# Kernel tuning notes

Hardware: AMD Instinct MI355X
Metric: run time of the kernel (lower is better)

## Reference

```python
import jax, jax.numpy as jnp
import numpy as np

LAMBDA_B = 5.0
N = 16_777_216  # 2^24 samples -> ~128 MB of fp32 inputs


def setup_inputs() -> dict:
    key = jax.random.key(0)
    k1, k2 = jax.random.split(key)
    y_true = jax.random.uniform(k1, (N,), dtype=jnp.float32)  # IWI-like scores in [0,1)
    y_pred = y_true + 0.1 * jax.random.normal(k2, (N,), dtype=jnp.float32)
    quants = jnp.arange(6, dtype=jnp.float32) / 5.0  # [0.0, 0.2, ..., 1.0]
    return {"y_pred": y_pred, "y_true": y_true, "quants": quants}


def reference(y_pred, y_true, quants):
    # MSE term
    diff = y_pred - y_true
    mse = jnp.mean(diff * diff)

    # Bucketize y_true into 5 bins: bin j is [q_j, q_{j+1}) for j<4, [q_4, q_5] for j=4.
    # searchsorted(side='right')-1 gives the half-open binning; values exactly equal
    # to quants[5] fall in the closed last bin; values outside [q0, q5] fall in no bin.
    idx = jnp.searchsorted(quants, y_true, side='right') - 1
    idx = jnp.where(y_true == quants[5], 4, idx)
    valid = (idx >= 0) & (idx <= 4)
    seg = jnp.where(valid, idx, 5).astype(jnp.int32)  # invalid -> dummy segment 5

    # Single-pass bucketized sum/count (the fused kernel this loss wants)
    sums = jax.ops.segment_sum(jnp.where(valid, diff, 0.0), seg, num_segments=6)
    counts = jax.ops.segment_sum(valid.astype(jnp.float32), seg, num_segments=6)

    bias = sums[:5] / jnp.maximum(counts[:5], 1.0)       # per-bin mean of (y_pred - y_true)
    bias2 = jnp.where(counts[:5] > 0, bias * bias, 0.0)  # empty bins contribute 0 (mask.any())
    max_bias2 = jnp.maximum(jnp.max(bias2), 0.0)         # torch starts from tensor(0.0)

    return mse + LAMBDA_B * max_bias2
```

## Files before the change

kernel.cpp:

```cpp
#include <hip/hip_runtime.h>
#include <math.h>

#define BLOCK 256
#define GRID 2048
#define FBLOCK 1024

__global__ __launch_bounds__(BLOCK) void ratledge_partial(
    const float* __restrict__ yp, const float* __restrict__ yt,
    const float* __restrict__ quants, float* __restrict__ partial, int n)
{
    float q[6];
#pragma unroll
    for (int j = 0; j < 6; ++j) q[j] = quants[j];
    const float q5 = q[5];

    float msum = 0.f;
    float ss[5] = {0.f, 0.f, 0.f, 0.f, 0.f};
    float sc[5] = {0.f, 0.f, 0.f, 0.f, 0.f};

    const int tid    = blockIdx.x * BLOCK + threadIdx.x;
    const int stride = GRID * BLOCK;
    const int n4     = n >> 2;
    const float4* yp4 = (const float4*)yp;
    const float4* yt4 = (const float4*)yt;

    auto body1 = [&](float p, float v) {
        float d = p - v;
        msum = fmaf(d, d, msum);
        float vv = (v <= q5) ? v : -INFINITY;
#pragma unroll
        for (int j = 0; j < 5; ++j) {
            bool m = (vv >= q[j]);
            ss[j] += m ? d   : 0.f;
            sc[j] += m ? 1.f : 0.f;
        }
    };
    auto body4 = [&](const float4& p, const float4& t) {
        body1(p.x, t.x); body1(p.y, t.y); body1(p.z, t.z); body1(p.w, t.w);
    };

    if (n == stride * 32) {
        float4 P[8], T[8];
#pragma unroll
        for (int r = 0; r < 8; ++r) {
            const int i = tid + r * stride;
            P[r] = yp4[i];
            T[r] = yt4[i];
        }
        __builtin_amdgcn_sched_barrier(0);
#pragma unroll
        for (int r = 0; r < 8; ++r)
            body4(P[r], T[r]);
    } else {
        const int trips = n4 / stride;
        for (int k = 0; k < trips; ++k) {
            const int i = tid + k * stride;
            float4 p = yp4[i];
            float4 t = yt4[i];
            body4(p, t);
        }
        const int i = tid + trips * stride;
        if (i < n4) {
            float4 p = yp4[i];
            float4 t = yt4[i];
            body4(p, t);
        }
        for (int i2 = (n4 << 2) + tid; i2 < n; i2 += stride)
            body1(yp[i2], yt[i2]);
    }

    float vals[11];
    vals[0] = msum;
#pragma unroll
    for (int j = 0; j < 5; ++j) { vals[1 + j] = ss[j]; vals[6 + j] = sc[j]; }
#pragma unroll
    for (int off = 32; off > 0; off >>= 1) {
#pragma unroll
        for (int j = 0; j < 11; ++j)
            vals[j] += __shfl_down(vals[j], off, 64);
    }

    __shared__ float sred[BLOCK / 64][11];
    const int lane = threadIdx.x & 63;
    const int wid  = threadIdx.x >> 6;
    if (lane == 0) {
#pragma unroll
        for (int j = 0; j < 11; ++j) sred[wid][j] = vals[j];
    }
    __syncthreads();
    if (threadIdx.x == 0) {
#pragma unroll
        for (int j = 0; j < 11; ++j) {
            float s = sred[0][j] + sred[1][j] + sred[2][j] + sred[3][j];
            partial[j * GRID + blockIdx.x] = s;
        }
    }
}

__global__ __launch_bounds__(FBLOCK) void ratledge_final(
    const float* __restrict__ partial, float* __restrict__ out, int n)
{
    const int t    = threadIdx.x;
    const int lane = t & 63;
    const int wid  = t >> 6;

    double acc[11];
#pragma unroll
    for (int j = 0; j < 11; ++j) {
        float a0 = partial[j * GRID + t];
        float a1 = partial[j * GRID + t + FBLOCK];
        acc[j] = (double)a0 + (double)a1;
    }

#pragma unroll
    for (int off = 32; off > 0; off >>= 1) {
#pragma unroll
        for (int j = 0; j < 11; ++j)
            acc[j] += __shfl_down(acc[j], off, 64);
    }

    __shared__ double sred[FBLOCK / 64][11];
    if (lane == 0) {
#pragma unroll
        for (int j = 0; j < 11; ++j) sred[wid][j] = acc[j];
    }
    __syncthreads();

    if (wid == 0) {
        double v[11];
#pragma unroll
        for (int j = 0; j < 11; ++j)
            v[j] = (lane < FBLOCK / 64) ? sred[lane][j] : 0.0;
#pragma unroll
        for (int off = 8; off > 0; off >>= 1) {
#pragma unroll
            for (int j = 0; j < 11; ++j)
                v[j] += __shfl_down(v[j], off, 64);
        }
        if (lane == 0) {
            double mse = v[0] / (double)n;
            double maxb2 = 0.0;
#pragma unroll
            for (int j = 0; j < 5; ++j) {
                double Sj  = v[1 + j];
                double Sj1 = (j < 4) ? v[2 + j] : 0.0;
                double Cj  = v[6 + j];
                double Cj1 = (j < 4) ? v[7 + j] : 0.0;
                double cnt = Cj - Cj1;
                double sum = Sj - Sj1;
                double bias = sum / fmax(cnt, 1.0);
                double b2   = (cnt > 0.0) ? bias * bias : 0.0;
                maxb2 = fmax(maxb2, b2);
            }
            out[0] = (float)(mse + 5.0 * maxb2);
        }
    }
}

extern "C" void kernel_launch(void* const* d_in, const int* in_sizes, int n_in,
                              void* d_out, int out_size, void* d_ws, size_t ws_size,
                              hipStream_t stream) {
    const float* yp = (const float*)d_in[0];
    const float* yt = (const float*)d_in[1];
    const float* q  = (const float*)d_in[2];
    float* partial  = (float*)d_ws;
    float* out      = (float*)d_out;
    int n = in_sizes[0];

    ratledge_partial<<<GRID, BLOCK, 0, stream>>>(yp, yt, q, partial, n);
    ratledge_final<<<1, FBLOCK, 0, stream>>>(partial, out, n);
}
```

Baseline: 156.1 us.

## Stream inputs through LDS with async global_load_lds triple buffering

Replaces the register-staged bulk load of eight float4 pairs with a three-deep ring of direct global-to-LDS loads, controlled by explicit vmcnt waits, so the next loads are in flight while the current tile is processed. The aim is to cut register pressure and keep memory requests overlapped with the binning arithmetic in this bandwidth-bound reduction. It adds 24 KB of LDS per block, which can limit occupancy, and relies on hand-written waitcnt ordering being correct.

```diff
diff --git a/kernel.cpp b/kernel.cpp
--- a/kernel.cpp
+++ b/kernel.cpp
@@ -4,11 +4,22 @@
 #define BLOCK 256
 #define GRID 2048
 #define FBLOCK 1024
+#define NTRIP 8
+
+__device__ __forceinline__ void gload_lds16(const float4* g, float4* l) {
+    __builtin_amdgcn_global_load_lds(
+        (const __attribute__((address_space(1))) void*)g,
+        (__attribute__((address_space(3))) void*)l,
+        16, 0, 0);
+}
 
 __global__ __launch_bounds__(BLOCK) void ratledge_partial(
     const float* __restrict__ yp, const float* __restrict__ yt,
     const float* __restrict__ quants, float* __restrict__ partial, int n)
 {
+    __shared__ float4 lA[3][BLOCK];
+    __shared__ float4 lB[3][BLOCK];
+
     float q[6];
 #pragma unroll
     for (int j = 0; j < 6; ++j) q[j] = quants[j];
@@ -39,18 +50,37 @@
         body1(p.x, t.x); body1(p.y, t.y); body1(p.z, t.z); body1(p.w, t.w);
     };
 
-    if (n == stride * 32) {
-        float4 P[8], T[8];
-#pragma unroll
-        for (int r = 0; r < 8; ++r) {
-            const int i = tid + r * stride;
-            P[r] = yp4[i];
-            T[r] = yt4[i];
-        }
-        __builtin_amdgcn_sched_barrier(0);
-#pragma unroll
-        for (int r = 0; r < 8; ++r)
-            body4(P[r], T[r]);
+    if (n == stride * (4 * NTRIP)) {
+        const int tx    = threadIdx.x;
+        const int wbase = tx & ~63;
+        const float4* gA = yp4 + tid;
+        const float4* gB = yt4 + tid;
+
+#pragma unroll
+        for (int k = 0; k < 3; ++k) {
+            gload_lds16(gA + k * stride, &lA[k][wbase]);
+            gload_lds16(gB + k * stride, &lB[k][wbase]);
+        }
+
+#pragma unroll
+        for (int k = 0; k < NTRIP; ++k) {
+            if (k <= NTRIP - 3)      asm volatile("s_waitcnt vmcnt(4)" ::: "memory");
+            else if (k == NTRIP - 2) asm volatile("s_waitcnt vmcnt(2)" ::: "memory");
+            else                     asm volatile("s_waitcnt vmcnt(0)" ::: "memory");
+            __builtin_amdgcn_sched_barrier(0);
+
+            float4 pv = lA[k % 3][tx];
+            float4 tv = lB[k % 3][tx];
+            asm volatile("s_waitcnt lgkmcnt(0)" ::: "memory");
+            __builtin_amdgcn_sched_barrier(0);
+
+            if (k + 3 < NTRIP) {
+                gload_lds16(gA + (k + 3) * stride, &lA[k % 3][wbase]);
+                gload_lds16(gB + (k + 3) * stride, &lB[k % 3][wbase]);
+            }
+
+            body4(pv, tv);
+        }
     } else {
         const int trips = n4 / stride;
         for (int k = 0; k < trips; ++k) {
```

Result: no change. 156.2 us (+0.1%).
